# Performance work log

Measured on AMD Instinct MI355X. Metric: run time of the kernel, lower is better.

## Reference

```python
import jax, jax.numpy as jnp
import numpy as np

L, H, D, F = 6, 8, 512, 2048
B, T, S = 8, 512, 1024
DK = D // H


def setup_inputs() -> dict:
    key = jax.random.key(0)
    ks = jax.random.split(key, 16)
    p = lambda k, shape: jax.random.normal(k, shape, jnp.float32) * 0.02
    inp = {
        "tgt": jax.random.normal(ks[0], (B, T, D), jnp.float32),
        "memory": jax.random.normal(ks[1], (B, S, D), jnp.float32),
        "source_mask": jnp.ones((B, 1, 1, S), jnp.int32),
        "target_mask": jnp.broadcast_to(jnp.tril(jnp.ones((T, T), jnp.int32)), (B, 1, T, T)),
        # self-attention params, stacked over layers
        "sa_wq": p(ks[2], (L, D, D)), "sa_wk": p(ks[3], (L, D, D)),
        "sa_wv": p(ks[4], (L, D, D)), "sa_wo": p(ks[5], (L, D, D)),
        "sa_bq": jnp.zeros((L, D)), "sa_bk": jnp.zeros((L, D)),
        "sa_bv": jnp.zeros((L, D)), "sa_bo": jnp.zeros((L, D)),
        # cross-attention params
        "ca_wq": p(ks[6], (L, D, D)), "ca_wk": p(ks[7], (L, D, D)),
        "ca_wv": p(ks[8], (L, D, D)), "ca_wo": p(ks[9], (L, D, D)),
        "ca_bq": jnp.zeros((L, D)), "ca_bk": jnp.zeros((L, D)),
        "ca_bv": jnp.zeros((L, D)), "ca_bo": jnp.zeros((L, D)),
        # FFN params
        "ff_w1": p(ks[10], (L, D, F)), "ff_b1": jnp.zeros((L, F)),
        "ff_w2": p(ks[11], (L, F, D)), "ff_b2": jnp.zeros((L, D)),
        # single shared LayerNorm (as in the original module)
        "ln_g": jnp.ones((D,)), "ln_b": jnp.zeros((D,)),
    }
    return inp


def _layernorm(x, g, b, eps=1e-5):
    m = jnp.mean(x, axis=-1, keepdims=True)
    v = jnp.var(x, axis=-1, keepdims=True)
    return (x - m) * jax.lax.rsqrt(v + eps) * g + b


def _mha(xq, xk, xv, wq, bq, wk, bk, wv, bv, wo, bo, mask):
    Bq = xq.shape[0]
    proj = lambda x, w, b: (x @ w + b).reshape(Bq, -1, H, DK).transpose(0, 2, 1, 3)
    q, k, v = proj(xq, wq, bq), proj(xk, wk, bk), proj(xv, wv, bv)  # [B,H,*,DK]
    scores = jnp.einsum('bhtd,bhsd->bhts', q, k) / jnp.sqrt(jnp.float32(DK))
    scores = jnp.where(mask == 0, jnp.float32(-1e9), scores)
    p_attn = jax.nn.softmax(scores, axis=-1)
    o = jnp.einsum('bhts,bhsd->bhtd', p_attn, v)
    o = o.transpose(0, 2, 1, 3).reshape(Bq, -1, H * DK)
    return o @ wo + bo


def reference(tgt, memory, source_mask, target_mask,
              sa_wq, sa_wk, sa_wv, sa_wo, sa_bq, sa_bk, sa_bv, sa_bo,
              ca_wq, ca_wk, ca_wv, ca_wo, ca_bq, ca_bk, ca_bv, ca_bo,
              ff_w1, ff_b1, ff_w2, ff_b2, ln_g, ln_b):
    output = tgt
    for i in range(L):
        # NOTE: faithful to original code: self-attn block uses `tgt`, not `output`
        n = _layernorm(tgt, ln_g, ln_b)
        output = tgt + _mha(n, n, n,
                            sa_wq[i], sa_bq[i], sa_wk[i], sa_bk[i],
                            sa_wv[i], sa_bv[i], sa_wo[i], sa_bo[i], target_mask)
        n = _layernorm(output, ln_g, ln_b)
        output = output + _mha(n, memory, memory,
                               ca_wq[i], ca_bq[i], ca_wk[i], ca_bk[i],
                               ca_wv[i], ca_bv[i], ca_wo[i], ca_bo[i], source_mask)
        n = _layernorm(output, ln_g, ln_b)
        ff = jax.nn.relu(n @ ff_w1[i] + ff_b1[i]) @ ff_w2[i] + ff_b2[i]
        output = output + ff
    return _layernorm(output, ln_g, ln_b)
```

## Files before the change

### kernel.cpp

```cpp
#include <hip/hip_runtime.h>

typedef __bf16 bf16;
typedef unsigned short u16;
typedef __bf16 bf16x8 __attribute__((ext_vector_type(8)));
typedef __bf16 bf16x4 __attribute__((ext_vector_type(4)));
typedef float f32x4 __attribute__((ext_vector_type(4)));

#define GLL16(gp, lp)                                                        \
    __builtin_amdgcn_global_load_lds(                                        \
        (const __attribute__((address_space(1))) void*)(gp),                 \
        (__attribute__((address_space(3))) void*)(lp), 16, 0, 0)

__device__ __forceinline__ bool is_f32(const void* lng_raw) {
    return ((const unsigned int*)lng_raw)[0] == 0x3F800000u;
}

__device__ __forceinline__ float ldf(const void* base, size_t idx, bool f32) {
    return f32 ? ((const float*)base)[idx] : (float)((const bf16*)base)[idx];
}

__device__ __forceinline__ uint4 load8(const void* base, size_t idx, bool f) {
    if (!f) return *(const uint4*)((const bf16*)base + idx);
    const float* p = (const float*)base + idx;
    float4 a = ((const float4*)p)[0], b = ((const float4*)p)[1];
    union { uint4 u; bf16 h[8]; } r;
    r.h[0] = (bf16)a.x; r.h[1] = (bf16)a.y; r.h[2] = (bf16)a.z; r.h[3] = (bf16)a.w;
    r.h[4] = (bf16)b.x; r.h[5] = (bf16)b.y; r.h[6] = (bf16)b.z; r.h[7] = (bf16)b.w;
    return r.u;
}

__global__ __launch_bounds__(256) void cvt_mem_k(const void* __restrict__ mem,
                                                 bf16* __restrict__ out,
                                                 const void* __restrict__ lng_raw) {
    size_t i = ((size_t)blockIdx.x * 256 + threadIdx.x) * 8;
    *(uint4*)(out + i) = load8(mem, i, is_f32(lng_raw));
}

__global__ void pack_vecs_k(const void* sbq, const void* sbk, const void* sbv,
                            const void* sbo, const void* cbq, const void* cbk,
                            const void* cbv, const void* cbo, const void* fb1,
                            const void* fb2, const void* lng, const void* lnb,
                            bf16* __restrict__ dst) {
    int i = blockIdx.x * 256 + threadIdx.x;
    bool f = is_f32(lng);
    const int L5D = 5 * 512, L5F = 5 * 2048;
    float v;
    if (i < 512) v = ldf(sbq, L5D + i, f);
    else if (i < 1024) v = ldf(sbk, L5D + i - 512, f);
    else if (i < 1536) v = ldf(sbv, L5D + i - 1024, f);
    else if (i < 2048) v = ldf(cbk, L5D + i - 1536, f);
    else if (i < 2560) v = ldf(cbv, L5D + i - 2048, f);
    else if (i < 3072) v = ldf(sbo, L5D + i - 2560, f);
    else if (i < 3584) v = ldf(cbq, L5D + i - 3072, f);
    else if (i < 4096) v = ldf(cbo, L5D + i - 3584, f);
    else if (i < 6144) v = ldf(fb1, L5F + i - 4096, f);
    else if (i < 6656) v = ldf(fb2, L5D + i - 6144, f);
    else if (i < 7168) v = ldf(lng, i - 6656, f);
    else v = ldf(lnb, i - 7168, f);
    dst[i] = (bf16)v;
}

struct SrcList { const void* p[10]; };
struct DstList { u16* p[10]; };
__global__ __launch_bounds__(256) void prep_w_k(SrcList SL, DstList DL,
                                                const void* __restrict__ lng) {
    __shared__ u16 tile[32][33];
    bool f = is_f32(lng);
    int t = blockIdx.x;
    int widx, R, C, tile_id;
    if (t < 2048) { widx = t >> 8; R = 512; C = 512; tile_id = t & 255; }
    else if (t < 3072) { widx = 8; R = 512; C = 2048; tile_id = t - 2048; }
    else { widx = 9; R = 2048; C = 512; tile_id = t - 3072; }
    int tpr = C >> 5;
    int cx = (tile_id % tpr) * 32, ry = (tile_id / tpr) * 32;
    size_t off = (widx < 8) ? (size_t)5 * 512 * 512 : (size_t)5 * 512 * 2048;
    const void* src = SL.p[widx];
    u16* dst = DL.p[widx];
    int tx = threadIdx.x & 31, ty = threadIdx.x >> 5;
#pragma unroll
    for (int i = 0; i < 32; i += 8) {
        bf16 bv = (bf16)ldf(src, off + (size_t)(ry + ty + i) * C + cx + tx, f);
        tile[ty + i][tx] = *(u16*)&bv;
    }
    __syncthreads();
#pragma unroll
    for (int i = 0; i < 32; i += 8)
        dst[(size_t)(cx + ty + i) * R + ry + tx] = tile[tx][ty + i];
}

__global__ __launch_bounds__(256) void vt2_k(const bf16* __restrict__ qkv,
                                             const bf16* __restrict__ kvca,
                                             bf16* __restrict__ vt_sa,
                                             bf16* __restrict__ vt_ca) {
    __shared__ u16 tile[32][33];
    int bid = blockIdx.x;
    const u16* src;
    u16* dst;
    int S, ld, coff, xs, ys, bh;
    if (bid < 2048) {
        src = (const u16*)qkv; dst = (u16*)vt_sa; S = 512; ld = 1536; coff = 1024;
        xs = bid & 15; ys = (bid >> 4) & 1; bh = bid >> 5;
    } else {
        int t = bid - 2048;
        src = (const u16*)kvca; dst = (u16*)vt_ca; S = 1024; ld = 1024; coff = 512;
        xs = t & 31; ys = (t >> 5) & 1; bh = t >> 6;
    }
    int b = bh >> 3, h = bh & 7;
    int s0 = xs * 32, d0 = ys * 32;
    int tx = threadIdx.x & 31, ty = threadIdx.x >> 5;
#pragma unroll
    for (int i = 0; i < 32; i += 8)
        tile[ty + i][tx] = src[(size_t)(b * S + s0 + ty + i) * ld + coff + h * 64 + d0 + tx];
    __syncthreads();
#pragma unroll
    for (int i = 0; i < 32; i += 8)
        dst[((size_t)bh * 64 + d0 + ty + i) * S + s0 + tx] = tile[tx][ty + i];
}

template <typename TIN>
__global__ __launch_bounds__(256) void ln_kernel(const TIN* __restrict__ x,
                                                 bf16* __restrict__ out,
                                                 const bf16* __restrict__ g,
                                                 const bf16* __restrict__ bb) {
    int row = blockIdx.x * 4 + (threadIdx.x >> 6);
    int lane = threadIdx.x & 63;
    const TIN* xr = x + (size_t)row * 512 + lane * 8;
    float v[8];
    if constexpr (sizeof(TIN) == 2) {
        uint4 u = *(const uint4*)xr;
        const bf16* p = (const bf16*)&u;
#pragma unroll
        for (int i = 0; i < 8; ++i) v[i] = (float)p[i];
    } else {
        float4 a = ((const float4*)xr)[0];
        float4 b2 = ((const float4*)xr)[1];
        v[0] = a.x; v[1] = a.y; v[2] = a.z; v[3] = a.w;
        v[4] = b2.x; v[5] = b2.y; v[6] = b2.z; v[7] = b2.w;
    }
    float s = 0.f, s2 = 0.f;
#pragma unroll
    for (int i = 0; i < 8; ++i) { s += v[i]; s2 += v[i] * v[i]; }
#pragma unroll
    for (int off = 32; off >= 1; off >>= 1) {
        s += __shfl_xor(s, off);
        s2 += __shfl_xor(s2, off);
    }
    float mean = s * (1.f / 512.f);
    float var = fmaxf(s2 * (1.f / 512.f) - mean * mean, 0.f);
    float rstd = rsqrtf(var + 1e-5f);
    int col = lane * 8;
    __align__(16) bf16 o8[8];
#pragma unroll
    for (int i = 0; i < 8; ++i)
        o8[i] = (bf16)((v[i] - mean) * rstd * (float)g[col + i] + (float)bb[col + i]);
    *(uint4*)(out + (size_t)row * 512 + col) = *(const uint4*)o8;
}

__global__ __launch_bounds__(256) void ln_raw_k(const void* __restrict__ x,
                                                bf16* __restrict__ out,
                                                const bf16* __restrict__ g,
                                                const bf16* __restrict__ bb,
                                                const void* __restrict__ lng_raw) {
    bool f = is_f32(lng_raw);
    int row = blockIdx.x * 4 + (threadIdx.x >> 6);
    int lane = threadIdx.x & 63;
    size_t base = (size_t)row * 512 + lane * 8;
    float v[8];
    if (f) {
        const float* xr = (const float*)x + base;
        float4 a = ((const float4*)xr)[0], b2 = ((const float4*)xr)[1];
        v[0] = a.x; v[1] = a.y; v[2] = a.z; v[3] = a.w;
        v[4] = b2.x; v[5] = b2.y; v[6] = b2.z; v[7] = b2.w;
    } else {
        uint4 u = *(const uint4*)((const bf16*)x + base);
        const bf16* p = (const bf16*)&u;
#pragma unroll
        for (int i = 0; i < 8; ++i) v[i] = (float)p[i];
    }
    float s = 0.f, s2 = 0.f;
#pragma unroll
    for (int i = 0; i < 8; ++i) { s += v[i]; s2 += v[i] * v[i]; }
#pragma unroll
    for (int off = 32; off >= 1; off >>= 1) {
        s += __shfl_xor(s, off);
        s2 += __shfl_xor(s2, off);
    }
    float mean = s * (1.f / 512.f);
    float var = fmaxf(s2 * (1.f / 512.f) - mean * mean, 0.f);
    float rstd = rsqrtf(var + 1e-5f);
    int col = lane * 8;
    __align__(16) bf16 o8[8];
#pragma unroll
    for (int i = 0; i < 8; ++i)
        o8[i] = (bf16)((v[i] - mean) * rstd * (float)g[col + i] + (float)bb[col + i]);
    *(uint4*)(out + (size_t)row * 512 + col) = *(const uint4*)o8;
}

__global__ __launch_bounds__(256) void ln_final_k(const float* __restrict__ x,
                                                  void* __restrict__ out,
                                                  const bf16* __restrict__ g,
                                                  const bf16* __restrict__ bb,
                                                  const void* __restrict__ lng_raw) {
    int row = blockIdx.x * 4 + (threadIdx.x >> 6);
    int lane = threadIdx.x & 63;
    const float* xr = x + (size_t)row * 512 + lane * 8;
    float v[8];
    float4 a = ((const float4*)xr)[0];
    float4 b2 = ((const float4*)xr)[1];
    v[0] = a.x; v[1] = a.y; v[2] = a.z; v[3] = a.w;
    v[4] = b2.x; v[5] = b2.y; v[6] = b2.z; v[7] = b2.w;
    float s = 0.f, s2 = 0.f;
#pragma unroll
    for (int i = 0; i < 8; ++i) { s += v[i]; s2 += v[i] * v[i]; }
#pragma unroll
    for (int off = 32; off >= 1; off >>= 1) {
        s += __shfl_xor(s, off);
        s2 += __shfl_xor(s2, off);
    }
    float mean = s * (1.f / 512.f);
    float var = fmaxf(s2 * (1.f / 512.f) - mean * mean, 0.f);
    float rstd = rsqrtf(var + 1e-5f);
    int col = lane * 8;
    float o[8];
#pragma unroll
    for (int i = 0; i < 8; ++i)
        o[i] = (v[i] - mean) * rstd * (float)g[col + i] + (float)bb[col + i];
    if (is_f32(lng_raw)) {
        float* op = (float*)out + (size_t)row * 512 + col;
        ((float4*)op)[0] = make_float4(o[0], o[1], o[2], o[3]);
        ((float4*)op)[1] = make_float4(o[4], o[5], o[6], o[7]);
    } else {
        __align__(16) bf16 o8[8];
#pragma unroll
        for (int i = 0; i < 8; ++i) o8[i] = (bf16)o[i];
        *(uint4*)((bf16*)out + (size_t)row * 512 + col) = *(const uint4*)o8;
    }
}

template <int TM, int RES, bool RELU, typename OUT_T>
__device__ __forceinline__ void gemm_body(const bf16* A, const bf16* Bt, const bf16* bias,
                                          const void* res, OUT_T* C,
                                          int K, int lda, int ldc,
                                          int m0, int n0, bool fR, bf16* lA, bf16* lB) {
    constexpr int MI = TM / 32;
    constexpr int AR = TM / 64;
    int tid = threadIdx.x;
    int w = tid >> 6, lane = tid & 63, quad = lane >> 4, c = lane & 15;
    int wm = (w >> 1) * (TM / 2), wn = (w & 1) * 64;
    f32x4 acc[MI][4] = {};

    auto issue = [&](int kt) {
#pragma unroll
        for (int r = 0; r < 2; ++r) {
            int id = r * 256 + tid;
            int rw = id >> 2, ch = id & 3;
            GLL16(&Bt[(size_t)(n0 + rw) * K + kt + ch * 8], &lB[id * 8]);
        }
#pragma unroll
        for (int r = 0; r < AR; ++r) {
            int id = r * 256 + tid;
            int rw = id >> 2, ch = id & 3;
            GLL16(&A[(size_t)(m0 + rw) * lda + kt + ch * 8], &lA[id * 8]);
        }
    };

    issue(0);
    __syncthreads();
    for (int kt = 0; kt < K; kt += 32) {
        bf16x8 af[MI], bfr[4];
#pragma unroll
        for (int i = 0; i < MI; ++i) af[i] = *(const bf16x8*)&lA[(wm + i * 16 + c) * 32 + quad * 8];
#pragma unroll
        for (int i = 0; i < 4; ++i) bfr[i] = *(const bf16x8*)&lB[(wn + i * 16 + c) * 32 + quad * 8];
        __syncthreads();
        if (kt + 32 < K) issue(kt + 32);
        __builtin_amdgcn_sched_barrier(0);
#pragma unroll
        for (int mi = 0; mi < MI; ++mi)
#pragma unroll
            for (int ni = 0; ni < 4; ++ni)
                acc[mi][ni] = __builtin_amdgcn_mfma_f32_16x16x32_bf16(
                    af[mi], bfr[ni], acc[mi][ni], 0, 0, 0);
        __syncthreads();
    }

#pragma unroll
    for (int mi = 0; mi < MI; ++mi) {
#pragma unroll
        for (int ni = 0; ni < 4; ++ni) {
#pragma unroll
            for (int r = 0; r < 4; ++r) {
                int row = m0 + wm + mi * 16 + quad * 4 + r;
                int col = n0 + wn + ni * 16 + c;
                float v = acc[mi][ni][r] + (float)bias[col];
                if (RELU) v = fmaxf(v, 0.f);
                if (RES == 1) v += ldf(res, (size_t)row * 512 + col, fR);
                if (RES == 2) v += ((const float*)res)[(size_t)row * 512 + col];
                C[(size_t)row * ldc + col] = (OUT_T)v;
            }
        }
    }
}

__global__ __launch_bounds__(256) void gemm_qkv_cakv(const bf16* __restrict__ nbuf,
                                                     const bf16* __restrict__ membf,
                                                     const bf16* __restrict__ wqkv,
                                                     const bf16* __restrict__ wcakv,
                                                     const bf16* __restrict__ cvec,
                                                     bf16* __restrict__ qkv,
                                                     bf16* __restrict__ kvca) {
    __shared__ __align__(16) bf16 lA[128 * 32];
    __shared__ __align__(16) bf16 lB[128 * 32];
    int bid = blockIdx.x;
    const bf16* A; const bf16* Bt; const bf16* bias; bf16* C;
    int ldc, m0, n0;
    if (bid < 384) {
        A = nbuf; Bt = wqkv; bias = cvec; C = qkv; ldc = 1536;
        m0 = (bid & 31) * 128; n0 = (bid >> 5) * 128;
    } else {
        int t = bid - 384;
        A = membf; Bt = wcakv; bias = cvec + 1536; C = kvca; ldc = 1024;
        m0 = (t & 63) * 128; n0 = (t >> 6) * 128;
    }
    gemm_body<128, 0, false, bf16>(A, Bt, bias, nullptr, C, 512, 512, ldc,
                                   m0, n0, false, lA, lB);
}

template <int TM, int RES, bool RELU, typename OUT_T>
__global__ __launch_bounds__(256) void gemmN(const bf16* __restrict__ A,
                                             const bf16* __restrict__ Bt,
                                             const bf16* __restrict__ bias,
                                             const void* __restrict__ res,
                                             OUT_T* __restrict__ C,
                                             int K, int lda, int ldc,
                                             const void* __restrict__ lng_raw) {
    __shared__ __align__(16) bf16 lA[TM * 32];
    __shared__ __align__(16) bf16 lB[128 * 32];
    bool f = (RES == 1) ? is_f32(lng_raw) : false;
    gemm_body<TM, RES, RELU, OUT_T>(A, Bt, bias, res, C, K, lda, ldc,
                                    blockIdx.x * TM, blockIdx.y * 128, f, lA, lB);
}

template <bool CAUSAL>
__global__ __launch_bounds__(256) void attn2_k(const bf16* __restrict__ Qb, int ldq,
                                               const bf16* __restrict__ Kb, int ldk,
                                               const bf16* __restrict__ Vt,
                                               const int* __restrict__ smask,
                                               bf16* __restrict__ O, int ldo,
                                               int Tq, int Skv) {
    __shared__ __align__(16) bf16 QPs[64 * 64];
    __shared__ __align__(16) bf16 Ks[64 * 64];
    __shared__ __align__(16) bf16 Vts[64 * 64];
    int tid = threadIdx.x;
    int bh = blockIdx.x, qt = blockIdx.y;
    int b = bh >> 3, h = bh & 7;
    int qbase = qt * 64, hoff = h * 64;
    int w = tid >> 6, lane = tid & 63, quad = lane >> 4, c = lane & 15;

#pragma unroll
    for (int r = 0; r < 2; ++r) {
        int id = r * 256 + tid;
        int rw = id >> 3, ch = id & 7;
        *(uint4*)&QPs[rw * 64 + ((ch ^ (rw & 7)) << 3)] =
            *(const uint4*)&Qb[(size_t)(b * Tq + qbase + rw) * ldq + hoff + ch * 8];
    }
    __syncthreads();
    bf16x8 qf[2];
    {
        int row = w * 16 + c;
        qf[0] = *(const bf16x8*)&QPs[row * 64 + ((quad ^ (row & 7)) << 3)];
        qf[1] = *(const bf16x8*)&QPs[row * 64 + (((4 + quad) ^ (row & 7)) << 3)];
    }

    float m_st = -1e4f, l_st = 0.f;
    f32x4 o_acc[4] = {};
    char* Pw = (char*)(QPs + w * 1024);

    int qg = qbase + w * 16 + c;
    int nkb = CAUSAL ? (qt + 1) : (Skv >> 6);

    for (int j = 0; j < nkb; ++j) {
        int kbase = j * 64;
        __syncthreads();
#pragma unroll
        for (int r = 0; r < 2; ++r) {
            int id = r * 256 + tid;
            int rw = id >> 3, ch = id & 7;
            int sw = (ch ^ (rw & 7)) << 3;
            *(uint4*)&Ks[rw * 64 + sw] =
                *(const uint4*)&Kb[(size_t)(b * Skv + kbase + rw) * ldk + hoff + ch * 8];
            *(uint4*)&Vts[rw * 64 + sw] =
                *(const uint4*)&Vt[((size_t)bh * 64 + rw) * Skv + kbase + ch * 8];
        }
        __syncthreads();

        f32x4 sv[4] = {};
#pragma unroll
        for (int ni = 0; ni < 4; ++ni) {
            int row = ni * 16 + c;
#pragma unroll
            for (int kk = 0; kk < 2; ++kk) {
                bf16x8 kf = *(const bf16x8*)&Ks[row * 64 + ((((kk << 2) + quad) ^ (row & 7)) << 3)];
                sv[ni] = __builtin_amdgcn_mfma_f32_16x16x32_bf16(kf, qf[kk], sv[ni], 0, 0, 0);
            }
        }

        float vv[4][4];
        float rm = -1e4f;
#pragma unroll
        for (int ni = 0; ni < 4; ++ni) {
            int kv0 = kbase + ni * 16 + quad * 4;
            if (CAUSAL) {
#pragma unroll
                for (int r = 0; r < 4; ++r) {
                    vv[ni][r] = (kv0 + r <= qg) ? sv[ni][r] * 0.125f : -1e4f;
                    rm = fmaxf(rm, vv[ni][r]);
                }
            } else {
                int4 mk = *(const int4*)&smask[b * Skv + kv0];
                const int* mp = (const int*)&mk;
#pragma unroll
                for (int r = 0; r < 4; ++r) {
                    vv[ni][r] = mp[r] ? sv[ni][r] * 0.125f : -1e4f;
                    rm = fmaxf(rm, vv[ni][r]);
                }
            }
        }
        rm = fmaxf(rm, __shfl_xor(rm, 16));
        rm = fmaxf(rm, __shfl_xor(rm, 32));
        float mn = fmaxf(m_st, rm);
        float alpha = __expf(m_st - mn);
        float rs = 0.f;
#pragma unroll
        for (int ni = 0; ni < 4; ++ni) {
            __align__(8) bf16 p4[4];
#pragma unroll
            for (int r = 0; r < 4; ++r) {
                float p = (vv[ni][r] > -9.9e3f) ? __expf(vv[ni][r] - mn) : 0.f;
                rs += p;
                p4[r] = (bf16)p;
            }
            int g = ni * 2 + (quad >> 1);
            *(bf16x4*)(Pw + c * 128 + ((g ^ (c & 7)) << 4) + (quad & 1) * 8) =
                *(const bf16x4*)p4;
        }
        rs += __shfl_xor(rs, 16);
        rs += __shfl_xor(rs, 32);
        l_st = l_st * alpha + rs;
        m_st = mn;
#pragma unroll
        for (int dt = 0; dt < 4; ++dt)
#pragma unroll
            for (int r = 0; r < 4; ++r) o_acc[dt][r] *= alpha;

        bf16x8 pf[2];
        pf[0] = *(const bf16x8*)(Pw + c * 128 + ((quad ^ (c & 7)) << 4));
        pf[1] = *(const bf16x8*)(Pw + c * 128 + (((4 + quad) ^ (c & 7)) << 4));
#pragma unroll
        for (int dt = 0; dt < 4; ++dt) {
            int row = dt * 16 + c;
#pragma unroll
            for (int kk = 0; kk < 2; ++kk) {
                bf16x8 vf = *(const bf16x8*)&Vts[row * 64 + ((((kk << 2) + quad) ^ (row & 7)) << 3)];
                o_acc[dt] = __builtin_amdgcn_mfma_f32_16x16x32_bf16(vf, pf[kk], o_acc[dt], 0, 0, 0);
            }
        }
    }

    float inv = 1.f / fmaxf(l_st, 1e-20f);
    size_t orow = (size_t)(b * Tq + qbase + w * 16 + c);
#pragma unroll
    for (int dt = 0; dt < 4; ++dt) {
        __align__(8) bf16 o4[4];
#pragma unroll
        for (int r = 0; r < 4; ++r) o4[r] = (bf16)(o_acc[dt][r] * inv);
        *(bf16x4*)&O[orow * ldo + hoff + dt * 16 + quad * 4] = *(const bf16x4*)o4;
    }
}

extern "C" void kernel_launch(void* const* d_in, const int* in_sizes, int n_in,
                              void* d_out, int out_size, void* d_ws, size_t ws_size,
                              hipStream_t stream) {
    (void)in_sizes; (void)n_in; (void)out_size; (void)ws_size;
    const size_t DD = (size_t)512 * 512;
    const int* smask = (const int*)d_in[2];
    const void* lng_raw = d_in[24];

    char* ws = (char*)d_ws;
    size_t off = 0;
    auto alloc = [&](size_t bytes) { void* p = ws + off; off += (bytes + 255) & ~(size_t)255; return p; };
    bf16* wt_qkv = (bf16*)alloc(1536 * 512 * 2);
    bf16* wt_sao = (bf16*)alloc(512 * 512 * 2);
    bf16* wt_caq = (bf16*)alloc(512 * 512 * 2);
    bf16* wt_cakv = (bf16*)alloc(1024 * 512 * 2);
    bf16* wt_cao = (bf16*)alloc(512 * 512 * 2);
    bf16* wt_ff1 = (bf16*)alloc(2048 * 512 * 2);
    bf16* wt_ff2 = (bf16*)alloc(512 * 2048 * 2);
    bf16* cvec = (bf16*)alloc(7680 * 2);
    bf16* membf = (bf16*)alloc((size_t)8192 * 512 * 2);
    bf16* nbuf = (bf16*)alloc((size_t)4096 * 512 * 2);
    bf16* attn = (bf16*)alloc((size_t)4096 * 512 * 2);
    bf16* qca = (bf16*)alloc((size_t)4096 * 512 * 2);
    float* x = (float*)alloc((size_t)4096 * 512 * 4);
    bf16* vt_sa = (bf16*)alloc((size_t)64 * 64 * 512 * 2);
    bf16* vt_ca = (bf16*)alloc((size_t)64 * 64 * 1024 * 2);
    bf16* kvca = (bf16*)alloc((size_t)8192 * 1024 * 2);
    bf16* big = (bf16*)alloc((size_t)4096 * 2048 * 2);
    bf16* qkv = big;
    bf16* hbuf = big;

    SrcList SL; DstList DL;
    SL.p[0] = d_in[4];  DL.p[0] = (u16*)wt_qkv;
    SL.p[1] = d_in[5];  DL.p[1] = (u16*)(wt_qkv + DD);
    SL.p[2] = d_in[6];  DL.p[2] = (u16*)(wt_qkv + 2 * DD);
    SL.p[3] = d_in[7];  DL.p[3] = (u16*)wt_sao;
    SL.p[4] = d_in[12]; DL.p[4] = (u16*)wt_caq;
    SL.p[5] = d_in[13]; DL.p[5] = (u16*)wt_cakv;
    SL.p[6] = d_in[14]; DL.p[6] = (u16*)(wt_cakv + DD);
    SL.p[7] = d_in[15]; DL.p[7] = (u16*)wt_cao;
    SL.p[8] = d_in[20]; DL.p[8] = (u16*)wt_ff1;
    SL.p[9] = d_in[22]; DL.p[9] = (u16*)wt_ff2;
    prep_w_k<<<4096, 256, 0, stream>>>(SL, DL, lng_raw);
    pack_vecs_k<<<30, 256, 0, stream>>>(d_in[8], d_in[9], d_in[10], d_in[11],
                                        d_in[16], d_in[17], d_in[18], d_in[19],
                                        d_in[21], d_in[23], d_in[24], d_in[25],
                                        cvec);
    cvt_mem_k<<<2048, 256, 0, stream>>>(d_in[1], membf, lng_raw);
    const bf16* lng = cvec + 6656;
    const bf16* lnb = cvec + 7168;

    ln_raw_k<<<1024, 256, 0, stream>>>(d_in[0], nbuf, lng, lnb, lng_raw);
    gemm_qkv_cakv<<<896, 256, 0, stream>>>(nbuf, membf, wt_qkv, wt_cakv, cvec,
                                           qkv, kvca);
    vt2_k<<<6144, 256, 0, stream>>>(qkv, kvca, vt_sa, vt_ca);

    attn2_k<true><<<dim3(64, 8), 256, 0, stream>>>(
        qkv, 1536, qkv + 512, 1536, vt_sa, nullptr, attn, 512, 512, 512);
    gemmN<64, 1, false, float><<<dim3(64, 4), 256, 0, stream>>>(
        attn, wt_sao, cvec + 2560, d_in[0], x, 512, 512, 512, lng_raw);

    ln_kernel<float><<<1024, 256, 0, stream>>>(x, nbuf, lng, lnb);
    gemmN<64, 0, false, bf16><<<dim3(64, 4), 256, 0, stream>>>(
        nbuf, wt_caq, cvec + 3072, nullptr, qca, 512, 512, 512, lng_raw);
    attn2_k<false><<<dim3(64, 8), 256, 0, stream>>>(
        qca, 512, kvca, 1024, vt_ca, smask, attn, 512, 512, 1024);
    gemmN<64, 2, false, float><<<dim3(64, 4), 256, 0, stream>>>(
        attn, wt_cao, cvec + 3584, x, x, 512, 512, 512, lng_raw);

    ln_kernel<float><<<1024, 256, 0, stream>>>(x, nbuf, lng, lnb);
    gemmN<128, 0, true, bf16><<<dim3(32, 16), 256, 0, stream>>>(
        nbuf, wt_ff1, cvec + 4096, nullptr, hbuf, 512, 512, 2048, lng_raw);
    gemmN<64, 2, false, float><<<dim3(64, 4), 256, 0, stream>>>(
        hbuf, wt_ff2, cvec + 6144, x, x, 2048, 2048, 512, lng_raw);

    ln_final_k<<<1024, 256, 0, stream>>>(x, d_out, lng, lnb, lng_raw);
}
```

Measured before the change: 359.3 us.

## Double-buffer K/V via async LDS loads and pair causal query tiles

The attention kernel now prefetches the next K/V tile into a second LDS buffer with global_load_lds while the current tile is being computed. The swizzle moves from the LDS write address to the global source address. For the causal case, each block handles query tile qt and 7-qt in turn, so every block does the same amount of work, and the grid is halved. This roughly doubles K/V shared memory and relies on correct wait counts for the async loads before each barrier.

```diff
diff --git a/kernel.cpp b/kernel.cpp
--- a/kernel.cpp
+++ b/kernel.cpp
@@ -349,132 +349,146 @@
                                                bf16* __restrict__ O, int ldo,
                                                int Tq, int Skv) {
     __shared__ __align__(16) bf16 QPs[64 * 64];
-    __shared__ __align__(16) bf16 Ks[64 * 64];
-    __shared__ __align__(16) bf16 Vts[64 * 64];
+    __shared__ __align__(16) bf16 Ks[2][64 * 64];
+    __shared__ __align__(16) bf16 Vts[2][64 * 64];
     int tid = threadIdx.x;
-    int bh = blockIdx.x, qt = blockIdx.y;
+    int bh = blockIdx.x;
     int b = bh >> 3, h = bh & 7;
-    int qbase = qt * 64, hoff = h * 64;
+    int hoff = h * 64;
     int w = tid >> 6, lane = tid & 63, quad = lane >> 4, c = lane & 15;
 
-#pragma unroll
-    for (int r = 0; r < 2; ++r) {
-        int id = r * 256 + tid;
-        int rw = id >> 3, ch = id & 7;
-        *(uint4*)&QPs[rw * 64 + ((ch ^ (rw & 7)) << 3)] =
-            *(const uint4*)&Qb[(size_t)(b * Tq + qbase + rw) * ldq + hoff + ch * 8];
-    }
-    __syncthreads();
-    bf16x8 qf[2];
-    {
-        int row = w * 16 + c;
-        qf[0] = *(const bf16x8*)&QPs[row * 64 + ((quad ^ (row & 7)) << 3)];
-        qf[1] = *(const bf16x8*)&QPs[row * 64 + (((4 + quad) ^ (row & 7)) << 3)];
-    }
-
-    float m_st = -1e4f, l_st = 0.f;
-    f32x4 o_acc[4] = {};
-    char* Pw = (char*)(QPs + w * 1024);
-
-    int qg = qbase + w * 16 + c;
-    int nkb = CAUSAL ? (qt + 1) : (Skv >> 6);
-
-    for (int j = 0; j < nkb; ++j) {
+    auto issueKV = [&](int j, int bs) {
         int kbase = j * 64;
+#pragma unroll
+        for (int rr = 0; rr < 2; ++rr) {
+            int id = rr * 256 + tid;
+            int rw = id >> 3, ch = id & 7;
+            int sg = (ch ^ (rw & 7)) << 3;
+            GLL16(&Kb[(size_t)(b * Skv + kbase + rw) * ldk + hoff + sg], &Ks[bs][id * 8]);
+            GLL16(&Vt[((size_t)bh * 64 + rw) * Skv + kbase + sg], &Vts[bs][id * 8]);
+        }
+    };
+
+    int nt = CAUSAL ? 2 : 1;
+    for (int t = 0; t < nt; ++t) {
+        int qt = CAUSAL ? (t ? 7 - (int)blockIdx.y : (int)blockIdx.y) : (int)blockIdx.y;
+        int qbase = qt * 64;
+        int nkb = CAUSAL ? (qt + 1) : (Skv >> 6);
+        int qg = qbase + w * 16 + c;
+
+        if (t) __syncthreads();
+#pragma unroll
+        for (int rr = 0; rr < 2; ++rr) {
+            int id = rr * 256 + tid;
+            int rw = id >> 3, ch = id & 7;
+            *(uint4*)&QPs[rw * 64 + ((ch ^ (rw & 7)) << 3)] =
+                *(const uint4*)&Qb[(size_t)(b * Tq + qbase + rw) * ldq + hoff + ch * 8];
+        }
+        issueKV(0, 0);
         __syncthreads();
-#pragma unroll
-        for (int r = 0; r < 2; ++r) {
-            int id = r * 256 + tid;
-            int rw = id >> 3, ch = id & 7;
-            int sw = (ch ^ (rw & 7)) << 3;
-            *(uint4*)&Ks[rw * 64 + sw] =
-                *(const uint4*)&Kb[(size_t)(b * Skv + kbase + rw) * ldk + hoff + ch * 8];
-            *(uint4*)&Vts[rw * 64 + sw] =
-                *(const uint4*)&Vt[((size_t)bh * 64 + rw) * Skv + kbase + ch * 8];
-        }
-        __syncthreads();
-
-        f32x4 sv[4] = {};
-#pragma unroll
-        for (int ni = 0; ni < 4; ++ni) {
-            int row = ni * 16 + c;
-#pragma unroll
-            for (int kk = 0; kk < 2; ++kk) {
-                bf16x8 kf = *(const bf16x8*)&Ks[row * 64 + ((((kk << 2) + quad) ^ (row & 7)) << 3)];
-                sv[ni] = __builtin_amdgcn_mfma_f32_16x16x32_bf16(kf, qf[kk], sv[ni], 0, 0, 0);
-            }
-        }
-
-        float vv[4][4];
-        float rm = -1e4f;
-#pragma unroll
-        for (int ni = 0; ni < 4; ++ni) {
-            int kv0 = kbase + ni * 16 + quad * 4;
-            if (CAUSAL) {
-#pragma unroll
-                for (int r = 0; r < 4; ++r) {
-                    vv[ni][r] = (kv0 + r <= qg) ? sv[ni][r] * 0.125f : -1e4f;
-                    rm = fmaxf(rm, vv[ni][r]);
-                }
-            } else {
-                int4 mk = *(const int4*)&smask[b * Skv + kv0];
-                const int* mp = (const int*)&mk;
-#pragma unroll
-                for (int r = 0; r < 4; ++r) {
-                    vv[ni][r] = mp[r] ? sv[ni][r] * 0.125f : -1e4f;
-                    rm = fmaxf(rm, vv[ni][r]);
+        bf16x8 qf[2];
+        {
+            int row = w * 16 + c;
+            qf[0] = *(const bf16x8*)&QPs[row * 64 + ((quad ^ (row & 7)) << 3)];
+            qf[1] = *(const bf16x8*)&QPs[row * 64 + (((4 + quad) ^ (row & 7)) << 3)];
+        }
+
+        float m_st = -1e4f, l_st = 0.f;
+        f32x4 o_acc[4] = {};
+        char* Pw = (char*)(QPs + w * 1024);
+
+        int cur = 0;
+        for (int j = 0; j < nkb; ++j) {
+            int kbase = j * 64;
+            if (j + 1 < nkb) issueKV(j + 1, cur ^ 1);
+            __builtin_amdgcn_sched_barrier(0);
+            const bf16* K_ = Ks[cur];
+            const bf16* V_ = Vts[cur];
+
+            f32x4 sv[4] = {};
+#pragma unroll
+            for (int ni = 0; ni < 4; ++ni) {
+                int row = ni * 16 + c;
+#pragma unroll
+                for (int kk = 0; kk < 2; ++kk) {
+                    bf16x8 kf = *(const bf16x8*)&K_[row * 64 + ((((kk << 2) + quad) ^ (row & 7)) << 3)];
+                    sv[ni] = __builtin_amdgcn_mfma_f32_16x16x32_bf16(kf, qf[kk], sv[ni], 0, 0, 0);
                 }
             }
-        }
-        rm = fmaxf(rm, __shfl_xor(rm, 16));
-        rm = fmaxf(rm, __shfl_xor(rm, 32));
-        float mn = fmaxf(m_st, rm);
-        float alpha = __expf(m_st - mn);
-        float rs = 0.f;
-#pragma unroll
-        for (int ni = 0; ni < 4; ++ni) {
-            __align__(8) bf16 p4[4];
-#pragma unroll
-            for (int r = 0; r < 4; ++r) {
-                float p = (vv[ni][r] > -9.9e3f) ? __expf(vv[ni][r] - mn) : 0.f;
-                rs += p;
-                p4[r] = (bf16)p;
+
+            float vv[4][4];
+            float rm = -1e4f;
+#pragma unroll
+            for (int ni = 0; ni < 4; ++ni) {
+                int kv0 = kbase + ni * 16 + quad * 4;
+                if (CAUSAL) {
+#pragma unroll
+                    for (int r = 0; r < 4; ++r) {
+                        vv[ni][r] = (kv0 + r <= qg) ? sv[ni][r] * 0.125f : -1e4f;
+                        rm = fmaxf(rm, vv[ni][r]);
+                    }
+                } else {
+                    int4 mk = *(const int4*)&smask[b * Skv + kv0];
+                    const int* mp = (const int*)&mk;
+#pragma unroll
+                    for (int r = 0; r < 4; ++r) {
+                        vv[ni][r] = mp[r] ? sv[ni][r] * 0.125f : -1e4f;
+                        rm = fmaxf(rm, vv[ni][r]);
+                    }
+                }
             }
-            int g = ni * 2 + (quad >> 1);
-            *(bf16x4*)(Pw + c * 128 + ((g ^ (c & 7)) << 4) + (quad & 1) * 8) =
-                *(const bf16x4*)p4;
-        }
-        rs += __shfl_xor(rs, 16);
-        rs += __shfl_xor(rs, 32);
-        l_st = l_st * alpha + rs;
-        m_st = mn;
-#pragma unroll
-        for (int dt = 0; dt < 4; ++dt)
-#pragma unroll
-            for (int r = 0; r < 4; ++r) o_acc[dt][r] *= alpha;
-
-        bf16x8 pf[2];
-        pf[0] = *(const bf16x8*)(Pw + c * 128 + ((quad ^ (c & 7)) << 4));
-        pf[1] = *(const bf16x8*)(Pw + c * 128 + (((4 + quad) ^ (c & 7)) << 4));
+            rm = fmaxf(rm, __shfl_xor(rm, 16));
+            rm = fmaxf(rm, __shfl_xor(rm, 32));
+            float mn = fmaxf(m_st, rm);
+            float alpha = __expf(m_st - mn);
+            float rs = 0.f;
+#pragma unroll
+            for (int ni = 0; ni < 4; ++ni) {
+                __align__(8) bf16 p4[4];
+#pragma unroll
+                for (int r = 0; r < 4; ++r) {
+                    float p = (vv[ni][r] > -9.9e3f) ? __expf(vv[ni][r] - mn) : 0.f;
+                    rs += p;
+                    p4[r] = (bf16)p;
+                }
+                int g = ni * 2 + (quad >> 1);
+                *(bf16x4*)(Pw + c * 128 + ((g ^ (c & 7)) << 4) + (quad & 1) * 8) =
+                    *(const bf16x4*)p4;
+            }
+            rs += __shfl_xor(rs, 16);
+            rs += __shfl_xor(rs, 32);
+            l_st = l_st * alpha + rs;
+            m_st = mn;
+#pragma unroll
+            for (int dt = 0; dt < 4; ++dt)
+#pragma unroll
+                for (int r = 0; r < 4; ++r) o_acc[dt][r] *= alpha;
+
+            bf16x8 pf[2];
+            pf[0] = *(const bf16x8*)(Pw + c * 128 + ((quad ^ (c & 7)) << 4));
+            pf[1] = *(const bf16x8*)(Pw + c * 128 + (((4 + quad) ^ (c & 7)) << 4));
+#pragma unroll
+            for (int dt = 0; dt < 4; ++dt) {
+                int row = dt * 16 + c;
+#pragma unroll
+                for (int kk = 0; kk < 2; ++kk) {
+                    bf16x8 vf = *(const bf16x8*)&V_[row * 64 + ((((kk << 2) + quad) ^ (row & 7)) << 3)];
+                    o_acc[dt] = __builtin_amdgcn_mfma_f32_16x16x32_bf16(vf, pf[kk], o_acc[dt], 0, 0, 0);
+                }
+            }
+            __syncthreads();
+            cur ^= 1;
+        }
+
+        float inv = 1.f / fmaxf(l_st, 1e-20f);
+        size_t orow = (size_t)(b * Tq + qbase + w * 16 + c);
 #pragma unroll
         for (int dt = 0; dt < 4; ++dt) {
-            int row = dt * 16 + c;
-#pragma unroll
-            for (int kk = 0; kk < 2; ++kk) {
-                bf16x8 vf = *(const bf16x8*)&Vts[row * 64 + ((((kk << 2) + quad) ^ (row & 7)) << 3)];
-                o_acc[dt] = __builtin_amdgcn_mfma_f32_16x16x32_bf16(vf, pf[kk], o_acc[dt], 0, 0, 0);
-            }
-        }
-    }
-
-    float inv = 1.f / fmaxf(l_st, 1e-20f);
-    size_t orow = (size_t)(b * Tq + qbase + w * 16 + c);
-#pragma unroll
-    for (int dt = 0; dt < 4; ++dt) {
-        __align__(8) bf16 o4[4];
-#pragma unroll
-        for (int r = 0; r < 4; ++r) o4[r] = (bf16)(o_acc[dt][r] * inv);
-        *(bf16x4*)&O[orow * ldo + hoff + dt * 16 + quad * 4] = *(const bf16x4*)o4;
+            __align__(8) bf16 o4[4];
+#pragma unroll
+            for (int r = 0; r < 4; ++r) o4[r] = (bf16)(o_acc[dt][r] * inv);
+            *(bf16x4*)&O[orow * ldo + hoff + dt * 16 + quad * 4] = *(const bf16x4*)o4;
+        }
     }
 }
 
@@ -534,7 +548,7 @@
                                            qkv, kvca);
     vt2_k<<<6144, 256, 0, stream>>>(qkv, kvca, vt_sa, vt_ca);
 
-    attn2_k<true><<<dim3(64, 8), 256, 0, stream>>>(
+    attn2_k<true><<<dim3(64, 4), 256, 0, stream>>>(
         qkv, 1536, qkv + 512, 1536, vt_sa, nullptr, attn, 512, 512, 512);
     gemmN<64, 1, false, float><<<dim3(64, 4), 256, 0, stream>>>(
         attn, wt_sao, cvec + 2560, d_in[0], x, 512, 512, 512, lng_raw);
```

Measured after the change: 356.6 us. Within noise of the previous version (-0.8%).
